# Kernel tuning notes

Measured on AMD Instinct MI355X. Metric: run time of the kernel, lower is better.

The kernel has to match this reference:

```python
import jax, jax.numpy as jnp
import numpy as np

N, IN, OUT = 8192, 4096, 16384


def setup_inputs() -> dict:
    key = jax.random.key(0)
    kx, kw, kb = jax.random.split(key, 3)
    x = jax.random.normal(kx, (N, IN), dtype=jnp.float32)
    # init matches reset_parameters: normal(0, sqrt(1/in_features))
    weight = jax.random.normal(kw, (OUT, IN), dtype=jnp.float32) * np.sqrt(1.0 / IN)
    bias = jax.random.normal(kb, (OUT,), dtype=jnp.float32) * 0.02
    return {"x": x, "weight": weight, "bias": bias}


def _ternarize(weight):
    # threshold = 0.5 * mean(|W|); zero out |w| < threshold, else sign(w)
    threshold = 0.5 * jnp.mean(jnp.abs(weight))
    keep = jnp.abs(weight) >= threshold
    ternary_weight = jnp.sign(weight) * keep.astype(weight.dtype)
    return ternary_weight


def reference(x, weight, bias):
    tw = _ternarize(weight)              # [out, in] in {-1, 0, 1}
    out = x @ tw.T + bias                # [N, out]
    return out
```

## Files before the change

### kernel.cpp

```cpp
#include <hip/hip_runtime.h>
#include <hip/hip_bf16.h>
#include <cstdint>
#include <cstddef>

#define M_DIM 8192
#define K_DIM 4096
#define N_DIM 16384

#define BM 256
#define BN 256
#define BK 32
#define NT (K_DIM / BK)
#define GX (N_DIM / BN)
#define GY (M_DIM / BM)
#define NWG (GX * GY)
#define CPX (NWG / 8)

typedef __attribute__((ext_vector_type(8))) short short8;
typedef __attribute__((ext_vector_type(4))) float floatx4;

__device__ inline void gl2lds16(const void* g, void* l) {
  __builtin_amdgcn_global_load_lds(
      (const __attribute__((address_space(1))) void*)g,
      (__attribute__((address_space(3))) void*)l, 16, 0, 0);
}

__global__ void abssum_kernel(const float* __restrict__ w, double* __restrict__ out) {
  size_t tid = (size_t)blockIdx.x * blockDim.x + threadIdx.x;
  size_t stride = (size_t)gridDim.x * blockDim.x;
  const float4* w4 = (const float4*)w;
  const size_t n4 = (size_t)N_DIM * K_DIM / 4;
  double s = 0.0;
  for (size_t i = tid; i < n4; i += stride) {
    float4 v = w4[i];
    s += (double)fabsf(v.x) + (double)fabsf(v.y) + (double)fabsf(v.z) + (double)fabsf(v.w);
  }
  #pragma unroll
  for (int off = 32; off > 0; off >>= 1) s += __shfl_down(s, off, 64);
  if ((threadIdx.x & 63) == 0) atomicAdd(out, s);
}

__global__ void ternarize_kernel(const float* __restrict__ w, ushort* __restrict__ tw,
                                 const double* __restrict__ sum) {
  const float thr = (float)(0.5 * (*sum) / (double)((size_t)N_DIM * K_DIM));
  size_t i = ((size_t)blockIdx.x * blockDim.x + threadIdx.x) * 8;
  float4 a = *(const float4*)(w + i);
  float4 b = *(const float4*)(w + i + 4);
  float v[8] = {a.x, a.y, a.z, a.w, b.x, b.y, b.z, b.w};
  union { ushort u[8]; uint4 q; } o;
  #pragma unroll
  for (int j = 0; j < 8; j++) {
    float av = fabsf(v[j]);
    o.u[j] = (av >= thr) ? ((v[j] > 0.0f) ? (ushort)0x3F80 : (ushort)0xBF80) : (ushort)0;
  }
  *(uint4*)(tw + i) = o.q;
}

__device__ inline ushort f2bf(float f) {
  uint32_t u = __float_as_uint(f);
  return (ushort)((u + 0x7FFFu + ((u >> 16) & 1u)) >> 16);
}
__global__ void bf16cast_kernel(const float* __restrict__ x, ushort* __restrict__ xb) {
  size_t i = ((size_t)blockIdx.x * blockDim.x + threadIdx.x) * 8;
  float4 a = *(const float4*)(x + i);
  float4 b = *(const float4*)(x + i + 4);
  float v[8] = {a.x, a.y, a.z, a.w, b.x, b.y, b.z, b.w};
  union { ushort u[8]; uint4 q; } o;
  #pragma unroll
  for (int j = 0; j < 8; j++) o.u[j] = f2bf(v[j]);
  *(uint4*)(xb + i) = o.q;
}

__global__ __launch_bounds__(512, 2)
void gemm_bt_kernel(const ushort* __restrict__ A, const ushort* __restrict__ B,
                    const float* __restrict__ bias, float* __restrict__ C) {
  __shared__ __align__(16) ushort As[4][BM * BK];
  __shared__ __align__(16) ushort Bs[4][BN * BK];

  const int tid  = threadIdx.x;
  const int wave = tid >> 6;
  const int lane = tid & 63;
  const int wm   = wave >> 2;
  const int wn   = wave & 3;
  const int r16  = lane & 15;
  const int quad = lane >> 4;

  const int flat = (int)(blockIdx.y * GX + blockIdx.x);
  const int swz  = (flat & 7) * CPX + (flat >> 3);
  const int bm   = swz / GX;
  const int bn   = swz % GX;

  const int srow = wave * 16 + (lane >> 2);
  const int scol = (lane & 3) * 8;
  const ushort* pA0 = A + (size_t)(bm * BM + srow) * K_DIM + scol;
  const ushort* pA1 = pA0 + (size_t)128 * K_DIM;
  const ushort* pB0 = B + (size_t)(bn * BN + srow) * K_DIM + scol;
  const ushort* pB1 = pB0 + (size_t)128 * K_DIM;
  const int ldsw = wave * 16 * BK;

#define STAGE_A(T) do { const int _b = (T) & 3;                        \
    gl2lds16(pA0 + (size_t)(T) * BK, &As[_b][ldsw]);                   \
    gl2lds16(pA1 + (size_t)(T) * BK, &As[_b][128 * BK + ldsw]); } while (0)
#define STAGE_B(T) do { const int _b = (T) & 3;                        \
    gl2lds16(pB0 + (size_t)(T) * BK, &Bs[_b][ldsw]);                   \
    gl2lds16(pB1 + (size_t)(T) * BK, &Bs[_b][128 * BK + ldsw]); } while (0)

  floatx4 acc[8][4];
  #pragma unroll
  for (int m = 0; m < 8; m++)
    #pragma unroll
    for (int n = 0; n < 4; n++)
      acc[m][n] = (floatx4){0.f, 0.f, 0.f, 0.f};

  STAGE_A(0); STAGE_B(0);
  STAGE_A(1); STAGE_B(1);
  STAGE_A(2); STAGE_B(2);
  STAGE_A(3);
  asm volatile("s_waitcnt vmcnt(10)" ::: "memory");
  __builtin_amdgcn_s_barrier();

  const int aoff = (wm * 128 + r16) * BK + quad * 8;
  const int boff = (wn * 64  + r16) * BK + quad * 8;

  for (int t = 0; t < NT; ++t) {
    const int cb = t & 3;
    short8 a[8], b[4];
    const ushort* aB = &As[cb][aoff];
    const ushort* bB = &Bs[cb][boff];
    #pragma unroll
    for (int m = 0; m < 8; ++m) a[m] = *(const short8*)(aB + m * 16 * BK);
    #pragma unroll
    for (int n = 0; n < 4; ++n) b[n] = *(const short8*)(bB + n * 16 * BK);
    if (t + 3 < NT) STAGE_B(t + 3);
    __builtin_amdgcn_s_barrier();
    asm volatile("s_waitcnt lgkmcnt(0)" ::: "memory");
    __builtin_amdgcn_sched_barrier(0);
    __builtin_amdgcn_s_setprio(1);
    #pragma unroll
    for (int m = 0; m < 4; ++m)
      #pragma unroll
      for (int n = 0; n < 4; ++n)
        acc[m][n] = __builtin_amdgcn_mfma_f32_16x16x32_bf16(a[m], b[n], acc[m][n], 0, 0, 0);
    __builtin_amdgcn_s_setprio(0);
    __builtin_amdgcn_s_barrier();
    if (t + 4 < NT) {
      STAGE_A(t + 4);
      asm volatile("s_waitcnt vmcnt(10)" ::: "memory");
    } else {
      asm volatile("s_waitcnt vmcnt(0)" ::: "memory");
    }
    __builtin_amdgcn_s_barrier();
    __builtin_amdgcn_s_setprio(1);
    #pragma unroll
    for (int m = 4; m < 8; ++m)
      #pragma unroll
      for (int n = 0; n < 4; ++n)
        acc[m][n] = __builtin_amdgcn_mfma_f32_16x16x32_bf16(a[m], b[n], acc[m][n], 0, 0, 0);
    __builtin_amdgcn_s_setprio(0);
    __builtin_amdgcn_s_barrier();
  }

  const int crow = bm * BM + wm * 128 + quad * 4;
  const int ccol = bn * BN + wn * 64 + r16;
  #pragma unroll
  for (int n = 0; n < 4; ++n) {
    const int col = ccol + n * 16;
    const float bv = bias[col];
    #pragma unroll
    for (int m = 0; m < 8; ++m) {
      const size_t row0 = (size_t)(crow + m * 16);
      #pragma unroll
      for (int r = 0; r < 4; ++r)
        C[(row0 + r) * N_DIM + col] = acc[m][n][r] + bv;
    }
  }
#undef STAGE_A
#undef STAGE_B
}

extern "C" void kernel_launch(void* const* d_in, const int* in_sizes, int n_in,
                              void* d_out, int out_size, void* d_ws, size_t ws_size,
                              hipStream_t stream) {
  const float* x    = (const float*)d_in[0];
  const float* w    = (const float*)d_in[1];
  const float* bias = (const float*)d_in[2];
  float* out = (float*)d_out;

  char* ws = (char*)d_ws;
  double* sum = (double*)ws;
  ushort* xb  = (ushort*)(ws + 256);
  ushort* tw  = (ushort*)(ws + 256 + (size_t)M_DIM * K_DIM * 2);

  hipMemsetAsync(sum, 0, sizeof(double), stream);
  abssum_kernel<<<2048, 256, 0, stream>>>(w, sum);
  ternarize_kernel<<<(size_t)N_DIM * K_DIM / 8 / 256, 256, 0, stream>>>(w, tw, sum);
  bf16cast_kernel<<<(size_t)M_DIM * K_DIM / 8 / 256, 256, 0, stream>>>(x, xb);

  dim3 grid(GX, GY);
  gemm_bt_kernel<<<grid, 512, 0, stream>>>(xb, tw, bias, out);
}
```

Measured before the change: 2.234 ms.

## Swizzle LDS layout, retile workgroup order, split LDS waits, nontemporal stores

Permutes which global rows and columns each lane stages into LDS so that the reads back out use an XOR-swizzled address, which is meant to remove LDS bank conflicts on the fragment loads. It also replaces the workgroup-to-tile mapping with a grouped 16x16-tile scheme to improve L2 reuse. The LDS wait is split so the first MFMA half only waits on the first fragment loads, letting the rest overlap. The output is written with nontemporal stores, and the ternarize threshold is computed once per block through shared memory. The swizzle must match exactly between the staging and the read side, or the GEMM results will be wrong.

```diff
diff --git a/kernel.cpp b/kernel.cpp
--- a/kernel.cpp
+++ b/kernel.cpp
@@ -13,8 +13,6 @@
 #define NT (K_DIM / BK)
 #define GX (N_DIM / BN)
 #define GY (M_DIM / BM)
-#define NWG (GX * GY)
-#define CPX (NWG / 8)
 
 typedef __attribute__((ext_vector_type(8))) short short8;
 typedef __attribute__((ext_vector_type(4))) float floatx4;
@@ -42,7 +40,11 @@
 
 __global__ void ternarize_kernel(const float* __restrict__ w, ushort* __restrict__ tw,
                                  const double* __restrict__ sum) {
-  const float thr = (float)(0.5 * (*sum) / (double)((size_t)N_DIM * K_DIM));
+  __shared__ float sthr;
+  if (threadIdx.x == 0)
+    sthr = (float)(0.5 * (*sum) / (double)((size_t)N_DIM * K_DIM));
+  __syncthreads();
+  const float thr = sthr;
   size_t i = ((size_t)blockIdx.x * blockDim.x + threadIdx.x) * 8;
   float4 a = *(const float4*)(w + i);
   float4 b = *(const float4*)(w + i + 4);
@@ -74,8 +76,8 @@
 __global__ __launch_bounds__(512, 2)
 void gemm_bt_kernel(const ushort* __restrict__ A, const ushort* __restrict__ B,
                     const float* __restrict__ bias, float* __restrict__ C) {
-  __shared__ __align__(16) ushort As[4][BM * BK];
-  __shared__ __align__(16) ushort Bs[4][BN * BK];
+  __shared__ __align__(128) ushort As[4][BM * BK];
+  __shared__ __align__(128) ushort Bs[4][BN * BK];
 
   const int tid  = threadIdx.x;
   const int wave = tid >> 6;
@@ -85,13 +87,22 @@
   const int r16  = lane & 15;
   const int quad = lane >> 4;
 
-  const int flat = (int)(blockIdx.y * GX + blockIdx.x);
-  const int swz  = (flat & 7) * CPX + (flat >> 3);
-  const int bm   = swz / GX;
-  const int bn   = swz % GX;
-
-  const int srow = wave * 16 + (lane >> 2);
-  const int scol = (lane & 3) * 8;
+  const int f  = (int)(blockIdx.y * GX + blockIdx.x);
+  const int xc = f & 7;
+  const int j  = f >> 3;
+  const int p  = j >> 5;
+  const int k  = j & 31;
+  const int pm = p >> 2, pn = p & 3;
+  const int bm = pm * 16 + ((xc >> 2) << 3) + (k & 7);
+  const int bn = pn * 16 + ((xc & 3) << 2) + (k >> 3);
+
+  const int bsw = ((lane >> 2) ^ (lane >> 4)) & 1;
+  const int rr  = ((lane >> 3) << 1) | bsw;
+  const int qb1 = ((lane >> 1) ^ (lane >> 3)) & 1;
+  const int qb0 = (lane ^ (lane >> 2) ^ (lane >> 4)) & 1;
+  const int qq  = (qb1 << 1) | qb0;
+  const int srow = wave * 16 + rr;
+  const int scol = qq * 8;
   const ushort* pA0 = A + (size_t)(bm * BM + srow) * K_DIM + scol;
   const ushort* pA1 = pA0 + (size_t)128 * K_DIM;
   const ushort* pB0 = B + (size_t)(bn * BN + srow) * K_DIM + scol;
@@ -119,21 +130,25 @@
   asm volatile("s_waitcnt vmcnt(10)" ::: "memory");
   __builtin_amdgcn_s_barrier();
 
-  const int aoff = (wm * 128 + r16) * BK + quad * 8;
-  const int boff = (wn * 64  + r16) * BK + quad * 8;
+  const int inner = ((r16 << 6) + (quad << 4)) ^ ((r16 & 7) << 4);
+  const char* aBytes; const char* bBytes;
 
   for (int t = 0; t < NT; ++t) {
     const int cb = t & 3;
+    aBytes = (const char*)(&As[cb][0]) + wm * 8192 + inner;
+    bBytes = (const char*)(&Bs[cb][0]) + wn * 4096 + inner;
     short8 a[8], b[4];
-    const ushort* aB = &As[cb][aoff];
-    const ushort* bB = &Bs[cb][boff];
-    #pragma unroll
-    for (int m = 0; m < 8; ++m) a[m] = *(const short8*)(aB + m * 16 * BK);
-    #pragma unroll
-    for (int n = 0; n < 4; ++n) b[n] = *(const short8*)(bB + n * 16 * BK);
+    #pragma unroll
+    for (int m = 0; m < 4; ++m) a[m] = *(const short8*)(aBytes + m * 1024);
+    #pragma unroll
+    for (int n = 0; n < 4; ++n) b[n] = *(const short8*)(bBytes + n * 1024);
+    __builtin_amdgcn_sched_barrier(0);
+    #pragma unroll
+    for (int m = 4; m < 8; ++m) a[m] = *(const short8*)(aBytes + m * 1024);
     if (t + 3 < NT) STAGE_B(t + 3);
-    __builtin_amdgcn_s_barrier();
-    asm volatile("s_waitcnt lgkmcnt(0)" ::: "memory");
+    __builtin_amdgcn_sched_barrier(0);
+    __builtin_amdgcn_s_barrier();
+    asm volatile("s_waitcnt lgkmcnt(4)" ::: "memory");
     __builtin_amdgcn_sched_barrier(0);
     __builtin_amdgcn_s_setprio(1);
     #pragma unroll
@@ -150,6 +165,8 @@
       asm volatile("s_waitcnt vmcnt(0)" ::: "memory");
     }
     __builtin_amdgcn_s_barrier();
+    asm volatile("s_waitcnt lgkmcnt(0)" ::: "memory");
+    __builtin_amdgcn_sched_barrier(0);
     __builtin_amdgcn_s_setprio(1);
     #pragma unroll
     for (int m = 4; m < 8; ++m)
@@ -171,7 +188,7 @@
       const size_t row0 = (size_t)(crow + m * 16);
       #pragma unroll
       for (int r = 0; r < 4; ++r)
-        C[(row0 + r) * N_DIM + col] = acc[m][n][r] + bv;
+        __builtin_nontemporal_store(acc[m][n][r] + bv, &C[(row0 + r) * N_DIM + col]);
     }
   }
 #undef STAGE_A
```

Result: faster. 1.998 ms (-10.6%).
